# Optimization experiments

Measured on AMD Instinct MI355X. Metric: run time of the kernel, lower is better.

Reference implementation:

```python
import jax, jax.numpy as jnp
import numpy as np

# Fixed production-scale sizes (equal-sized graphs so unbatch == reshape)
B, NQ, ND = 64, 32, 512     # graph pairs, query nodes/graph, data nodes/graph
DIN, D, K = 64, 128, 16     # GCN_in_size, GCN_out_size, NTN_k
DEG = 8                     # average degree


def _gcn(x, src, dst, W, b):
    """GCNConv with self loops + symmetric normalization (PyG semantics)."""
    N = x.shape[0]
    loop = jnp.arange(N)
    s = jnp.concatenate([src, loop])
    t = jnp.concatenate([dst, loop])
    deg = jax.ops.segment_sum(jnp.ones_like(t, x.dtype), t, num_segments=N)
    dinv = jnp.where(deg > 0, deg ** -0.5, 0.0)
    norm = (dinv[s] * dinv[t])[:, None]
    h = x @ W
    return jax.ops.segment_sum(h[s] * norm, t, num_segments=N) + b


def _three_gcn(x, ei, W1, b1, W2, b2, W3, b3):
    src, dst = ei[0], ei[1]
    h1 = jax.nn.relu(_gcn(x, src, dst, W1, b1))
    h2 = jax.nn.relu(_gcn(h1, src, dst, W2, b2))
    h3 = jax.nn.relu(_gcn(h2, src, dst, W3, b3))
    return h1, h2, h3


def _level(q, d, Wn, Vn, bn, cw, cb):
    """att_layer + NTN + elementwise mult + 1x1 conv + softmax over data nodes.
    q: [B,NQ,D], d: [B,ND,D] -> (softmaxed map [B,NQ,ND], raw map, he [B,K,NQ,ND])."""
    att = jax.nn.softmax(jnp.einsum('bqd,bnd->bqn', q, d) / jnp.sqrt(jnp.float32(D)), axis=-1)
    qW = jnp.einsum('bqd,kde->bkqe', q, Wn)           # [B,K,NQ,D]
    bil = jnp.einsum('bkqe,bne->bkqn', qW, d)          # [B,K,NQ,ND]
    lq = jnp.einsum('kd,bqd->bkq', Vn[:, :D], q)[:, :, :, None]
    ld = jnp.einsum('kd,bnd->bkn', Vn[:, D:], d)[:, :, None, :]
    he = jax.nn.sigmoid(bil + lq + ld + bn[None, :, None, None]) * att[:, None]
    e_raw = jnp.einsum('k,bkqn->bqn', cw, he) + cb     # 1x1 Conv2d(K->1)
    return jax.nn.softmax(e_raw, axis=-1), e_raw, he


def reference(x_d, edge_index_d, x_q, edge_index_q, batch_index_d, batch_index_q,
              W1, b1, W2, b2, W3, b3,
              Wn1, Vn1, bn1, cw1, cb1,
              Wn2, Vn2, bn2, cw2, cb2,
              Wn3, Vn3, bn3, cw3, cb3,
              w_end, b_end):
    d1, d2, d3 = _three_gcn(x_d, edge_index_d, W1, b1, W2, b2, W3, b3)
    q1, q2, q3 = _three_gcn(x_q, edge_index_q, W1, b1, W2, b2, W3, b3)
    # unbatch: batch indices are sorted with equal graph sizes -> reshape
    d1, d2, d3 = (t.reshape(B, ND, D) for t in (d1, d2, d3))
    q1, q2, q3 = (t.reshape(B, NQ, D) for t in (q1, q2, q3))
    e1, _, he1 = _level(q1, d1, Wn1, Vn1, bn1, cw1, cb1)
    _, e2raw, he2 = _level(q2, d2, Wn2, Vn2, bn2, cw2, cb2)
    e3, _, he3 = _level(q3, d3, Wn3, Vn3, bn3, cw3, cb3)
    # Faithful to source quirks: the zip unpack `e1,e2,e3,h1,h2,h1` rebinds h1 to
    # he_3 (he_1 is never used, he_3 appears twice) and end2 enters the concat
    # PRE-softmax (the softmaxed version was assigned to unused `nd2`).
    stack = jnp.concatenate([e1[:, None], e2raw[:, None], e3[:, None], he3, he2, he3], axis=1)
    out = jnp.einsum('c,bcqn->bqn', w_end, stack) + b_end  # con_end 1x1 conv + squeeze
    return jax.nn.softmax(out, axis=-1)                    # softmax over data nodes


def setup_inputs() -> dict:
    key = jax.random.key(0)
    k = jax.random.split(key, 40)
    n = jax.random.normal
    Nd, Nq = B * ND, B * NQ
    Ed, Eq = Nd * DEG, Nq * DEG
    gid_d = jnp.repeat(jnp.arange(B), ND * DEG)
    gid_q = jnp.repeat(jnp.arange(B), NQ * DEG)
    inp = {
        'x_d': n(k[0], (Nd, DIN), jnp.float32),
        'x_q': n(k[1], (Nq, DIN), jnp.float32),
        'edge_index_d': jnp.stack([jax.random.randint(k[2], (Ed,), 0, ND) + gid_d * ND,
                                   jax.random.randint(k[3], (Ed,), 0, ND) + gid_d * ND]),
        'edge_index_q': jnp.stack([jax.random.randint(k[4], (Eq,), 0, NQ) + gid_q * NQ,
                                   jax.random.randint(k[5], (Eq,), 0, NQ) + gid_q * NQ]),
        'batch_index_d': jnp.repeat(jnp.arange(B), ND),
        'batch_index_q': jnp.repeat(jnp.arange(B), NQ),
        'W1': n(k[6], (DIN, D), jnp.float32) / np.sqrt(DIN), 'b1': jnp.zeros((D,), jnp.float32),
        'W2': n(k[7], (D, D), jnp.float32) / np.sqrt(D), 'b2': jnp.zeros((D,), jnp.float32),
        'W3': n(k[8], (D, D), jnp.float32) / np.sqrt(D), 'b3': jnp.zeros((D,), jnp.float32),
    }
    for i, l in enumerate(('1', '2', '3')):
        inp['Wn' + l] = n(k[10 + 4 * i], (K, D, D), jnp.float32) / np.sqrt(D)
        inp['Vn' + l] = n(k[11 + 4 * i], (K, 2 * D), jnp.float32) / np.sqrt(2 * D)
        inp['bn' + l] = jnp.zeros((K,), jnp.float32)
        inp['cw' + l] = n(k[12 + 4 * i], (K,), jnp.float32) / np.sqrt(K)
        inp['cb' + l] = jnp.zeros((1,), jnp.float32)
    inp['w_end'] = n(k[25], (3 * K + 3,), jnp.float32) / np.sqrt(3 * K + 3)
    inp['b_end'] = jnp.zeros((1,), jnp.float32)
    return inp
```

## Files before the change

kernel.cpp:

```cpp
#include <hip/hip_runtime.h>
#include <math.h>

namespace {
constexpr int cB  = 64;
constexpr int cNQ = 32;
constexpr int cND = 512;
constexpr int cNd = cB * cND;
constexpr int cNq = cB * cNQ;
constexpr int cEd = cNd * 8;
constexpr int cEq = cNq * 8;
constexpr int LD_STRIDE = 516;
constexpr int NB_CVT = 2188, NB_T2BF = 808, NB_CNT = (cEd + cEq) / 256;
constexpr int NB_FILL = (cEd + cEq) / 256;
}

#define F4C(p) (*(const float4*)(p))

typedef __attribute__((ext_vector_type(8))) __bf16 bf16x8;
typedef __attribute__((ext_vector_type(4))) float floatx4;

__device__ __forceinline__ ushort f2bf(float f) {
  union { float f; unsigned u; } v;
  v.f = f;
  unsigned u = v.u;
  return (ushort)((u + 0x7fffu + ((u >> 16) & 1u)) >> 16);
}
__device__ __forceinline__ float bf2f(ushort u) {
  union { unsigned u; float f; } v;
  v.u = ((unsigned)u) << 16;
  return v.f;
}
__device__ __forceinline__ float4 us4f4(ushort4 u) {
  return make_float4(bf2f(u.x), bf2f(u.y), bf2f(u.z), bf2f(u.w));
}
__device__ __forceinline__ ushort4 f4us4(float4 f) {
  ushort4 o;
  o.x = f2bf(f.x); o.y = f2bf(f.y); o.z = f2bf(f.z); o.w = f2bf(f.w);
  return o;
}
__device__ __forceinline__ float fexp2(float x) {
#if __has_builtin(__builtin_amdgcn_exp2f)
  return __builtin_amdgcn_exp2f(x);
#else
  return exp2f(x);
#endif
}
__device__ __forceinline__ float frcp(float x) {
#if __has_builtin(__builtin_amdgcn_rcpf)
  return __builtin_amdgcn_rcpf(x);
#else
  return 1.0f / x;
#endif
}
__device__ __forceinline__ float fsigmoid(float z) {
  return frcp(1.0f + fexp2(z * -1.4426950408889634f));
}
__device__ __forceinline__ float fexp(float x) { return fexp2(x * 1.4426950408889634f); }

template <int L>
__device__ __forceinline__ int swzg(int j) { return ((j >> (3 + L)) << 3) | (j & 7); }
template <int L>
__device__ __forceinline__ int swzs(int j) { return (j >> 3) & ((1 << L) - 1); }

__global__ __launch_bounds__(256) void k_front(
    const float* __restrict__ xd, const float* __restrict__ xq,
    const float* __restrict__ v0, const float* __restrict__ v1,
    const float* __restrict__ v2, ushort* __restrict__ oxd, ushort* __restrict__ oxq,
    ushort* __restrict__ ov0, ushort* __restrict__ ov1, ushort* __restrict__ ov2,
    const float* __restrict__ W1, const float* __restrict__ W2,
    const float* __restrict__ W3, const float* __restrict__ Wn0,
    const float* __restrict__ Wn1, const float* __restrict__ Wn2,
    ushort* __restrict__ o1, ushort* __restrict__ o2, ushort* __restrict__ o3,
    ushort* __restrict__ on0, ushort* __restrict__ on1, ushort* __restrict__ on2,
    const int* __restrict__ dst_d, const int* __restrict__ dst_q,
    int* __restrict__ cnt_d, int* __restrict__ cnt_q) {
  __shared__ float tile[32][33];
  int blk = blockIdx.x, tid = threadIdx.x;
  if (blk < NB_CVT) {
    const float* src;
    ushort* dst;
    int i;
    if (blk < 2048) { src = xd; dst = oxd; i = blk * 256 + tid; }
    else if (blk < 2176) { src = xq; dst = oxq; i = (blk - 2048) * 256 + tid; }
    else if (blk < 2180) { src = v0; dst = ov0; i = (blk - 2176) * 256 + tid; }
    else if (blk < 2184) { src = v1; dst = ov1; i = (blk - 2180) * 256 + tid; }
    else { src = v2; dst = ov2; i = (blk - 2184) * 256 + tid; }
    *(ushort4*)(dst + (size_t)i * 4) = f4us4(F4C(src + (size_t)i * 4));
  } else if (blk < NB_CVT + NB_T2BF) {
    int b5 = blk - NB_CVT;
    const float* in;
    ushort* out;
    int R, C, bt, t;
    if (b5 < 8)        { in = W1;  out = o1;  R = 64;  C = 128; bt = 0; t = b5; }
    else if (b5 < 24)  { in = W2;  out = o2;  R = 128; C = 128; bt = 0; t = b5 - 8; }
    else if (b5 < 40)  { in = W3;  out = o3;  R = 128; C = 128; bt = 0; t = b5 - 24; }
    else if (b5 < 296) { in = Wn0; out = on0; R = 128; C = 128; bt = (b5 - 40) >> 4;  t = (b5 - 40) & 15; }
    else if (b5 < 552) { in = Wn1; out = on1; R = 128; C = 128; bt = (b5 - 296) >> 4; t = (b5 - 296) & 15; }
    else               { in = Wn2; out = on2; R = 128; C = 128; bt = (b5 - 552) >> 4; t = (b5 - 552) & 15; }
    int tilesC = C >> 5;
    int tr = t / tilesC, tc = t - tr * tilesC;
    int tx = tid & 31, ty = tid >> 5;
    const float* ib = in + (size_t)bt * R * C;
    ushort* ob = out + (size_t)bt * R * C;
#pragma unroll
    for (int i = 0; i < 4; ++i)
      tile[ty + i * 8][tx] = ib[(tr * 32 + ty + i * 8) * C + tc * 32 + tx];
    __syncthreads();
#pragma unroll
    for (int i = 0; i < 4; ++i)
      ob[(size_t)(tc * 32 + ty + i * 8) * R + tr * 32 + tx] = f2bf(tile[tx][ty + i * 8]);
  } else {
    int i = (blk - NB_CVT - NB_T2BF) * 256 + tid;
    if (i < cEd) atomicAdd(&cnt_d[dst_d[i]], 1);
    else atomicAdd(&cnt_q[dst_q[i - cEd]], 1);
  }
}

__global__ __launch_bounds__(512) void k_scan_dinv(
    const int* __restrict__ cnt_d, const int* __restrict__ cnt_q,
    int* __restrict__ rp_d, int* __restrict__ rp_q,
    float* __restrict__ dinv_d, float* __restrict__ dinv_q) {
  __shared__ int sh[512];
  int blk = blockIdx.x, tid = threadIdx.x;
  if (blk < 64) {
    int v = cnt_d[blk * 512 + tid];
    sh[tid] = v;
    __syncthreads();
    for (int off = 1; off < 512; off <<= 1) {
      int t = (tid >= off) ? sh[tid - off] : 0;
      __syncthreads();
      sh[tid] += t;
      __syncthreads();
    }
    rp_d[blk * 512 + tid] = blk * 4096 + sh[tid] - v;
  } else if (blk < 68) {
    int g = (blk - 64) * 16 + (tid >> 5);
    int lane32 = tid & 31;
    int v = cnt_q[g * 32 + lane32];
    int incl = v;
#pragma unroll
    for (int off = 1; off < 32; off <<= 1) {
      int t = __shfl_up(incl, off, 32);
      if (lane32 >= off) incl += t;
    }
    rp_q[g * 32 + lane32] = g * 256 + incl - v;
  } else {
    int i = (blk - 68) * 512 + tid;
    if (i < cNd) dinv_d[i] = 1.0f / sqrtf((float)(cnt_d[i] + 1));
    else dinv_q[i - cNd] = 1.0f / sqrtf((float)(cnt_q[i - cNd] + 1));
  }
}

__global__ __launch_bounds__(256) void k_fill_gemm1(
    const int* __restrict__ src_d, const int* __restrict__ dst_d,
    const int* __restrict__ src_q, const int* __restrict__ dst_q,
    const int* __restrict__ rp_d, const int* __restrict__ rp_q,
    int* __restrict__ cur_d, int* __restrict__ cur_q, int* __restrict__ col_d,
    int* __restrict__ col_q, const ushort* __restrict__ xdbf,
    const ushort* __restrict__ xqbf, const ushort* __restrict__ w1T,
    const float* __restrict__ dinv_d, const float* __restrict__ dinv_q,
    ushort* __restrict__ htmp) {
  int blk = blockIdx.x, tid = threadIdx.x;
  if (blk < NB_FILL) {
    int i = blk * 256 + tid;
    if (i < cEd) {
      int d = dst_d[i];
      int p = atomicAdd(&cur_d[d], 1);
      col_d[rp_d[d] + p] = src_d[i];
    } else {
      int j = i - cEd;
      int d = dst_q[j];
      int p = atomicAdd(&cur_q[d], 1);
      col_q[rp_q[d] + p] = src_q[j];
    }
    return;
  }
  int blk2 = blk - NB_FILL;
  int wave = tid >> 6, lane = tid & 63;
  int col = lane & 15, quad = lane >> 4;
  bool isQ = blk2 >= 512;
  int node0;
  if (isQ) node0 = (blk2 - 512) * 64;
  else node0 = swzg<3>(blk2) * 512 + swzs<3>(blk2) * 64;
  int mloc = node0 + wave * 16;
  const ushort* X = isQ ? xqbf : xdbf;
  const float* dv = isQ ? dinv_q : dinv_d;
  size_t hbase = isQ ? (size_t)cNd : 0;
  floatx4 acc[8];
#pragma unroll
  for (int ct = 0; ct < 8; ++ct)
#pragma unroll
    for (int r = 0; r < 4; ++r) acc[ct][r] = 0.0f;
#pragma unroll
  for (int kc = 0; kc < 2; ++kc) {
    bf16x8 a = *(const bf16x8*)(X + (size_t)(mloc + col) * 64 + kc * 32 + quad * 8);
#pragma unroll
    for (int ct = 0; ct < 8; ++ct) {
      bf16x8 b = *(const bf16x8*)(w1T + (size_t)(ct * 16 + col) * 64 + kc * 32 + quad * 8);
      acc[ct] = __builtin_amdgcn_mfma_f32_16x16x32_bf16(a, b, acc[ct], 0, 0, 0);
    }
  }
  float sc[4];
#pragma unroll
  for (int r = 0; r < 4; ++r) sc[r] = dv[mloc + quad * 4 + r];
#pragma unroll
  for (int ct = 0; ct < 8; ++ct)
#pragma unroll
    for (int r = 0; r < 4; ++r)
      htmp[(hbase + mloc + quad * 4 + r) * 128 + ct * 16 + col] = f2bf(acc[ct][r] * sc[r]);
}

__global__ __launch_bounds__(256) void gmn_gather_merged(
    const ushort* __restrict__ htmp, const int* __restrict__ rp_d,
    const int* __restrict__ cnt_d, const int* __restrict__ col_d,
    const float* __restrict__ dinv_d, const int* __restrict__ rp_q,
    const int* __restrict__ cnt_q, const int* __restrict__ col_q,
    const float* __restrict__ dinv_q, const float* __restrict__ bias,
    ushort* __restrict__ dbf, ushort* __restrict__ qbf) {
  int blk = blockIdx.x, tid = threadIdx.x;
  bool isQ = blk >= 4096;
  int node;
  if (isQ) {
    int j = blk - 4096;
    node = swzg<2>(j) * 32 + swzs<2>(j) * 8 + (tid >> 5);
  } else {
    node = swzg<6>(blk) * 512 + swzs<6>(blk) * 8 + (tid >> 5);
  }
  int l = tid & 31;
  const ushort* hs = htmp + (isQ ? (size_t)cNd * 128 : 0);
  const int* rp = isQ ? rp_q : rp_d;
  const int* cnt = isQ ? cnt_q : cnt_d;
  const int* col = isQ ? col_q : col_d;
  const float* dinv = isQ ? dinv_q : dinv_d;
  ushort* outp = isQ ? qbf : dbf;
  int c = cnt[node], s0 = rp[node];
  float dt = dinv[node];
  float4 acc = us4f4(*(const ushort4*)(hs + (size_t)node * 128 + l * 4));
  int cm = c < 32 ? c : 32;
  for (int j0 = 0; j0 < cm; j0 += 8) {
    int ss[8];
    ushort4 v[8];
#pragma unroll
    for (int t = 0; t < 8; ++t) {
      int jj = j0 + t;
      ss[t] = (jj < cm) ? col[s0 + jj] : -1;
    }
#pragma unroll
    for (int t = 0; t < 8; ++t)
      if (ss[t] >= 0) v[t] = *(const ushort4*)(hs + (size_t)ss[t] * 128 + l * 4);
#pragma unroll
    for (int t = 0; t < 8; ++t) {
      if (ss[t] >= 0) {
        float4 f = us4f4(v[t]);
        acc.x += f.x; acc.y += f.y; acc.z += f.z; acc.w += f.w;
      }
    }
  }
  for (int j = 32; j < c; ++j) {
    int s = col[s0 + j];
    float4 f = us4f4(*(const ushort4*)(hs + (size_t)s * 128 + l * 4));
    acc.x += f.x; acc.y += f.y; acc.z += f.z; acc.w += f.w;
  }
  float4 bv = F4C(bias + l * 4);
  float4 r;
  r.x = fmaxf(acc.x * dt + bv.x, 0.0f);
  r.y = fmaxf(acc.y * dt + bv.y, 0.0f);
  r.z = fmaxf(acc.z * dt + bv.z, 0.0f);
  r.w = fmaxf(acc.w * dt + bv.w, 0.0f);
  *(ushort4*)(outp + (size_t)node * 128 + l * 4) = f4us4(r);
}

__global__ __launch_bounds__(256) void gmn_qw(const ushort* __restrict__ qbf,
                                              const ushort* __restrict__ wnT,
                                              ushort* __restrict__ qw) {
  int blk = blockIdx.x, tid = threadIdx.x;
  int wave = tid >> 6, lane = tid & 63;
  int col = lane & 15, quad = lane >> 4;
  int b = swzg<4>(blk), k = swzs<4>(blk);
  int et0 = wave * 2;
  floatx4 acc[2][2];
#pragma unroll
  for (int qt = 0; qt < 2; ++qt)
#pragma unroll
    for (int ei = 0; ei < 2; ++ei)
#pragma unroll
      for (int r = 0; r < 4; ++r) acc[qt][ei][r] = 0.0f;
#pragma unroll
  for (int kc = 0; kc < 4; ++kc) {
    bf16x8 a0 = *(const bf16x8*)(qbf + (size_t)(b * 32 + col) * 128 + kc * 32 + quad * 8);
    bf16x8 a1 = *(const bf16x8*)(qbf + (size_t)(b * 32 + 16 + col) * 128 + kc * 32 + quad * 8);
#pragma unroll
    for (int ei = 0; ei < 2; ++ei) {
      bf16x8 bf = *(const bf16x8*)(wnT + (size_t)(k * 128 + (et0 + ei) * 16 + col) * 128 +
                                   kc * 32 + quad * 8);
      acc[0][ei] = __builtin_amdgcn_mfma_f32_16x16x32_bf16(a0, bf, acc[0][ei], 0, 0, 0);
      acc[1][ei] = __builtin_amdgcn_mfma_f32_16x16x32_bf16(a1, bf, acc[1][ei], 0, 0, 0);
    }
  }
#pragma unroll
  for (int qt = 0; qt < 2; ++qt)
#pragma unroll
    for (int ei = 0; ei < 2; ++ei)
#pragma unroll
      for (int r = 0; r < 4; ++r)
        qw[((size_t)(b * 16 + k) << 12) + (qt * 16 + quad * 4 + r) * 128 +
           (et0 + ei) * 16 + col] = f2bf(acc[qt][ei][r]);
}

__global__ __launch_bounds__(512, 2) void k_level_gemm(
    const ushort* __restrict__ qbf, const ushort* __restrict__ dbf,
    const ushort* __restrict__ qw, const ushort* __restrict__ vnbf,
    const float* __restrict__ bn, const float* __restrict__ cw,
    const float* __restrict__ w_end, const float* __restrict__ b_end,
    int o1, int o2, int hasF, int do_sm, int mode, int widx,
    float* __restrict__ accb, float* __restrict__ out,
    const ushort* __restrict__ gWT, const float* __restrict__ dinv_d,
    const float* __restrict__ dinv_q, ushort* __restrict__ htmp) {
  __shared__ float s_ld[16 * LD_STRIDE];
  __shared__ float s_lq[16 * 16];
  __shared__ float s_red[16 * 8];
  int tid = threadIdx.x;
  int wave = tid >> 6, lane = tid & 63;
  int col = lane & 15, quad = lane >> 4;

  if (blockIdx.x >= 128) {
    int gblk = blockIdx.x - 128;
    bool isQ = gblk >= 256;
    int node0;
    if (isQ) node0 = (gblk - 256) * 128;
    else node0 = swzg<2>(gblk) * 512 + swzs<2>(gblk) * 128;
    int mloc = node0 + wave * 16;
    const ushort* X = isQ ? qbf : dbf;
    const float* dv = isQ ? dinv_q : dinv_d;
    size_t hbase = isQ ? (size_t)cNd : 0;
    floatx4 acc[8];
#pragma unroll
    for (int ct = 0; ct < 8; ++ct)
#pragma unroll
      for (int r = 0; r < 4; ++r) acc[ct][r] = 0.0f;
#pragma unroll
    for (int kc = 0; kc < 4; ++kc) {
      bf16x8 a = *(const bf16x8*)(X + (size_t)(mloc + col) * 128 + kc * 32 + quad * 8);
#pragma unroll
      for (int ct = 0; ct < 8; ++ct) {
        bf16x8 b = *(const bf16x8*)(gWT + (size_t)(ct * 16 + col) * 128 + kc * 32 + quad * 8);
        acc[ct] = __builtin_amdgcn_mfma_f32_16x16x32_bf16(a, b, acc[ct], 0, 0, 0);
      }
    }
    float sc[4];
#pragma unroll
    for (int r = 0; r < 4; ++r) sc[r] = dv[mloc + quad * 4 + r];
#pragma unroll
    for (int ct = 0; ct < 8; ++ct)
#pragma unroll
      for (int r = 0; r < 4; ++r)
        htmp[(hbase + mloc + quad * 4 + r) * 128 + ct * 16 + col] = f2bf(acc[ct][r] * sc[r]);
    return;
  }

  int b = swzg<1>(blockIdx.x);
  int qh = swzs<1>(blockIdx.x);
  int n0 = wave * 64;

  bf16x8 bfr[4][4];
#pragma unroll
  for (int s = 0; s < 4; ++s)
#pragma unroll
    for (int kc = 0; kc < 4; ++kc)
      bfr[s][kc] = *(const bf16x8*)(dbf + ((size_t)(b * 512 + n0 + s * 16 + col) << 7) +
                                    kc * 32 + quad * 8);
  bf16x8 aq[4];
#pragma unroll
  for (int kc = 0; kc < 4; ++kc)
    aq[kc] = *(const bf16x8*)(qbf + (size_t)(b * 32 + qh * 16 + col) * 128 +
                              kc * 32 + quad * 8);

  floatx4 att[4];
#pragma unroll
  for (int s = 0; s < 4; ++s)
#pragma unroll
    for (int r = 0; r < 4; ++r) att[s][r] = 0.0f;
#pragma unroll
  for (int kc = 0; kc < 4; ++kc)
#pragma unroll
    for (int s = 0; s < 4; ++s)
      att[s] = __builtin_amdgcn_mfma_f32_16x16x32_bf16(aq[kc], bfr[s][kc], att[s], 0, 0, 0);
  const float sc = 0.088388347648318440550f;
#pragma unroll
  for (int s = 0; s < 4; ++s)
#pragma unroll
    for (int r = 0; r < 4; ++r) att[s][r] *= sc;

  {
    bf16x8 vn2[4];
#pragma unroll
    for (int kc = 0; kc < 4; ++kc)
      vn2[kc] = *(const bf16x8*)(vnbf + col * 256 + 128 + kc * 32 + quad * 8);
#pragma unroll
    for (int s = 0; s < 4; ++s) {
      floatx4 lda;
#pragma unroll
      for (int r = 0; r < 4; ++r) lda[r] = 0.0f;
#pragma unroll
      for (int kc = 0; kc < 4; ++kc)
        lda = __builtin_amdgcn_mfma_f32_16x16x32_bf16(bfr[s][kc], vn2[kc], lda, 0, 0, 0);
#pragma unroll
      for (int r = 0; r < 4; ++r)
        s_ld[col * LD_STRIDE + n0 + s * 16 + quad * 4 + r] = lda[r];
    }
  }
  if (wave == 0) {
    bf16x8 vn1[4];
#pragma unroll
    for (int kc = 0; kc < 4; ++kc)
      vn1[kc] = *(const bf16x8*)(vnbf + col * 256 + kc * 32 + quad * 8);
    floatx4 lqa;
#pragma unroll
    for (int r = 0; r < 4; ++r) lqa[r] = 0.0f;
#pragma unroll
    for (int kc = 0; kc < 4; ++kc)
      lqa = __builtin_amdgcn_mfma_f32_16x16x32_bf16(aq[kc], vn1[kc], lqa, 0, 0, 0);
#pragma unroll
    for (int r = 0; r < 4; ++r) s_lq[col * 16 + quad * 4 + r] = lqa[r];
  }
  __syncthreads();

  float red[4], M[4];
#pragma unroll
  for (int r = 0; r < 4; ++r) {
    float m = fmaxf(fmaxf(att[0][r], att[1][r]), fmaxf(att[2][r], att[3][r]));
#pragma unroll
    for (int o = 1; o < 16; o <<= 1) m = fmaxf(m, __shfl_xor(m, o, 64));
    red[r] = m;
  }
  if (col == 0)
#pragma unroll
    for (int r = 0; r < 4; ++r) s_red[(quad * 4 + r) * 8 + wave] = red[r];
  __syncthreads();
#pragma unroll
  for (int r = 0; r < 4; ++r) {
    float m = s_red[(quad * 4 + r) * 8];
#pragma unroll
    for (int w = 1; w < 8; ++w) m = fmaxf(m, s_red[(quad * 4 + r) * 8 + w]);
    M[r] = m;
  }
  __syncthreads();
#pragma unroll
  for (int s = 0; s < 4; ++s)
#pragma unroll
    for (int r = 0; r < 4; ++r) att[s][r] = fexp(att[s][r] - M[r]);
#pragma unroll
  for (int r = 0; r < 4; ++r) {
    float m = att[0][r] + att[1][r] + att[2][r] + att[3][r];
#pragma unroll
    for (int o = 1; o < 16; o <<= 1) m += __shfl_xor(m, o, 64);
    red[r] = m;
  }
  if (col == 0)
#pragma unroll
    for (int r = 0; r < 4; ++r) s_red[(quad * 4 + r) * 8 + wave] = red[r];
  __syncthreads();
#pragma unroll
  for (int r = 0; r < 4; ++r) {
    float m = s_red[(quad * 4 + r) * 8];
#pragma unroll
    for (int w = 1; w < 8; ++w) m += s_red[(quad * 4 + r) * 8 + w];
    M[r] = frcp(m);
  }
  __syncthreads();
#pragma unroll
  for (int s = 0; s < 4; ++s)
#pragma unroll
    for (int r = 0; r < 4; ++r) att[s][r] *= M[r];

  floatx4 eacc[4], facc[4];
#pragma unroll
  for (int s = 0; s < 4; ++s)
#pragma unroll
    for (int r = 0; r < 4; ++r) { eacc[s][r] = 0.0f; facc[s][r] = 0.0f; }

#pragma unroll 4
  for (int k = 0; k < 16; ++k) {
    const ushort* qk = qw + ((size_t)(b * 16 + k) << 12) + (qh * 16 + col) * 128 + quad * 8;
    bf16x8 a0 = *(const bf16x8*)(qk);
    bf16x8 a1 = *(const bf16x8*)(qk + 32);
    bf16x8 a2 = *(const bf16x8*)(qk + 64);
    bf16x8 a3 = *(const bf16x8*)(qk + 96);
    floatx4 bil[4];
#pragma unroll
    for (int s = 0; s < 4; ++s) {
#pragma unroll
      for (int r = 0; r < 4; ++r) bil[s][r] = 0.0f;
      bil[s] = __builtin_amdgcn_mfma_f32_16x16x32_bf16(a0, bfr[s][0], bil[s], 0, 0, 0);
      bil[s] = __builtin_amdgcn_mfma_f32_16x16x32_bf16(a1, bfr[s][1], bil[s], 0, 0, 0);
      bil[s] = __builtin_amdgcn_mfma_f32_16x16x32_bf16(a2, bfr[s][2], bil[s], 0, 0, 0);
      bil[s] = __builtin_amdgcn_mfma_f32_16x16x32_bf16(a3, bfr[s][3], bil[s], 0, 0, 0);
    }
    float bnk = bn[k], cwk = cw[k];
    float wkk = 0.0f;
    if (hasF) {
      wkk = w_end[o1 + k];
      if (o2 >= 0) wkk += w_end[o2 + k];
    }
    float lqv[4];
#pragma unroll
    for (int r = 0; r < 4; ++r) lqv[r] = s_lq[k * 16 + quad * 4 + r] + bnk;
#pragma unroll
    for (int s = 0; s < 4; ++s) {
      float ldv = s_ld[k * LD_STRIDE + n0 + s * 16 + col];
#pragma unroll
      for (int r = 0; r < 4; ++r) {
        float sg = fsigmoid(bil[s][r] + lqv[r] + ldv);
        eacc[s][r] += cwk * sg;
        facc[s][r] += wkk * sg;
      }
    }
  }

#pragma unroll
  for (int s = 0; s < 4; ++s)
#pragma unroll
    for (int r = 0; r < 4; ++r) {
      eacc[s][r] *= att[s][r];
      facc[s][r] *= att[s][r];
    }
  if (do_sm) {
#pragma unroll
    for (int r = 0; r < 4; ++r) {
      float m = fmaxf(fmaxf(eacc[0][r], eacc[1][r]), fmaxf(eacc[2][r], eacc[3][r]));
#pragma unroll
      for (int o = 1; o < 16; o <<= 1) m = fmaxf(m, __shfl_xor(m, o, 64));
      red[r] = m;
    }
    if (col == 0)
#pragma unroll
      for (int r = 0; r < 4; ++r) s_red[(quad * 4 + r) * 8 + wave] = red[r];
    __syncthreads();
#pragma unroll
    for (int r = 0; r < 4; ++r) {
      float m = s_red[(quad * 4 + r) * 8];
#pragma unroll
      for (int w = 1; w < 8; ++w) m = fmaxf(m, s_red[(quad * 4 + r) * 8 + w]);
      M[r] = m;
    }
    __syncthreads();
#pragma unroll
    for (int s = 0; s < 4; ++s)
#pragma unroll
      for (int r = 0; r < 4; ++r) eacc[s][r] = fexp(eacc[s][r] - M[r]);
#pragma unroll
    for (int r = 0; r < 4; ++r) {
      float m = eacc[0][r] + eacc[1][r] + eacc[2][r] + eacc[3][r];
#pragma unroll
      for (int o = 1; o < 16; o <<= 1) m += __shfl_xor(m, o, 64);
      red[r] = m;
    }
    if (col == 0)
#pragma unroll
      for (int r = 0; r < 4; ++r) s_red[(quad * 4 + r) * 8 + wave] = red[r];
    __syncthreads();
#pragma unroll
    for (int r = 0; r < 4; ++r) {
      float m = s_red[(quad * 4 + r) * 8];
#pragma unroll
      for (int w = 1; w < 8; ++w) m += s_red[(quad * 4 + r) * 8 + w];
      M[r] = frcp(m);
    }
    __syncthreads();
#pragma unroll
    for (int s = 0; s < 4; ++s)
#pragma unroll
      for (int r = 0; r < 4; ++r) eacc[s][r] *= M[r];
  }
  float w = w_end[widx];
#pragma unroll
  for (int s = 0; s < 4; ++s)
#pragma unroll
    for (int r = 0; r < 4; ++r) eacc[s][r] = w * eacc[s][r] + (hasF ? facc[s][r] : 0.0f);

  if (mode == 0) {
#pragma unroll
    for (int s = 0; s < 4; ++s)
#pragma unroll
      for (int r = 0; r < 4; ++r)
        accb[((size_t)(b * 32 + qh * 16 + quad * 4 + r) << 9) + n0 + s * 16 + col] =
            eacc[s][r];
  } else if (mode == 1) {
#pragma unroll
    for (int s = 0; s < 4; ++s)
#pragma unroll
      for (int r = 0; r < 4; ++r)
        accb[((size_t)(b * 32 + qh * 16 + quad * 4 + r) << 9) + n0 + s * 16 + col] +=
            eacc[s][r];
  } else {
    float be = b_end[0];
#pragma unroll
    for (int s = 0; s < 4; ++s)
#pragma unroll
      for (int r = 0; r < 4; ++r)
        eacc[s][r] += accb[((size_t)(b * 32 + qh * 16 + quad * 4 + r) << 9) +
                           n0 + s * 16 + col] + be;
#pragma unroll
    for (int r = 0; r < 4; ++r) {
      float m = fmaxf(fmaxf(eacc[0][r], eacc[1][r]), fmaxf(eacc[2][r], eacc[3][r]));
#pragma unroll
      for (int o = 1; o < 16; o <<= 1) m = fmaxf(m, __shfl_xor(m, o, 64));
      red[r] = m;
    }
    if (col == 0)
#pragma unroll
      for (int r = 0; r < 4; ++r) s_red[(quad * 4 + r) * 8 + wave] = red[r];
    __syncthreads();
#pragma unroll
    for (int r = 0; r < 4; ++r) {
      float m = s_red[(quad * 4 + r) * 8];
#pragma unroll
      for (int w2 = 1; w2 < 8; ++w2) m = fmaxf(m, s_red[(quad * 4 + r) * 8 + w2]);
      M[r] = m;
    }
    __syncthreads();
#pragma unroll
    for (int s = 0; s < 4; ++s)
#pragma unroll
      for (int r = 0; r < 4; ++r) eacc[s][r] = fexp(eacc[s][r] - M[r]);
#pragma unroll
    for (int r = 0; r < 4; ++r) {
      float m = eacc[0][r] + eacc[1][r] + eacc[2][r] + eacc[3][r];
#pragma unroll
      for (int o = 1; o < 16; o <<= 1) m += __shfl_xor(m, o, 64);
      red[r] = m;
    }
    if (col == 0)
#pragma unroll
      for (int r = 0; r < 4; ++r) s_red[(quad * 4 + r) * 8 + wave] = red[r];
    __syncthreads();
#pragma unroll
    for (int r = 0; r < 4; ++r) {
      float m = s_red[(quad * 4 + r) * 8];
#pragma unroll
      for (int w2 = 1; w2 < 8; ++w2) m += s_red[(quad * 4 + r) * 8 + w2];
      M[r] = frcp(m);
    }
#pragma unroll
    for (int s = 0; s < 4; ++s)
#pragma unroll
      for (int r = 0; r < 4; ++r)
        out[((size_t)(b * 32 + qh * 16 + quad * 4 + r) << 9) + n0 + s * 16 + col] =
            eacc[s][r] * M[r];
  }
}

extern "C" void kernel_launch(void* const* d_in, const int* in_sizes, int n_in,
                              void* d_out, int out_size, void* d_ws, size_t ws_size,
                              hipStream_t stream) {
  (void)in_sizes; (void)n_in; (void)out_size; (void)ws_size;
  const float* x_d = (const float*)d_in[0];
  const float* x_q = (const float*)d_in[1];
  const int* ei_d = (const int*)d_in[2];
  const int* ei_q = (const int*)d_in[3];
  const float* W1 = (const float*)d_in[6];
  const float* b1 = (const float*)d_in[7];
  const float* W2 = (const float*)d_in[8];
  const float* b2 = (const float*)d_in[9];
  const float* W3 = (const float*)d_in[10];
  const float* b3 = (const float*)d_in[11];
  const float* Wn[3] = {(const float*)d_in[12], (const float*)d_in[17], (const float*)d_in[22]};
  const float* Vn[3] = {(const float*)d_in[13], (const float*)d_in[18], (const float*)d_in[23]};
  const float* bn[3] = {(const float*)d_in[14], (const float*)d_in[19], (const float*)d_in[24]};
  const float* cw[3] = {(const float*)d_in[15], (const float*)d_in[20], (const float*)d_in[25]};
  const float* w_end = (const float*)d_in[27];
  const float* b_end = (const float*)d_in[28];
  float* out = (float*)d_out;

  char* wsp = (char*)d_ws;
  auto alloc = [&](size_t nbytes) {
    void* p = (void*)wsp;
    wsp += (nbytes + 255) & ~(size_t)255;
    return p;
  };
  int* cnt_d = (int*)alloc(cNd * 4);
  int* cnt_q = (int*)alloc(cNq * 4);
  int* cur_d = (int*)alloc(cNd * 4);
  int* cur_q = (int*)alloc(cNq * 4);
  float* dinv_d = (float*)alloc(cNd * 4);
  float* dinv_q = (float*)alloc(cNq * 4);
  int* rp_d = (int*)alloc(cNd * 4);
  int* rp_q = (int*)alloc(cNq * 4);
  int* col_d = (int*)alloc((size_t)cEd * 4);
  int* col_q = (int*)alloc((size_t)cEq * 4);
  ushort* xdbf = (ushort*)alloc((size_t)cNd * 64 * 2);
  ushort* xqbf = (ushort*)alloc((size_t)cNq * 64 * 2);
  ushort* w1T = (ushort*)alloc(128 * 64 * 2);
  ushort* w2T = (ushort*)alloc(128 * 128 * 2);
  ushort* w3T = (ushort*)alloc(128 * 128 * 2);
  ushort* wnT[3];
  for (int l = 0; l < 3; ++l) wnT[l] = (ushort*)alloc((size_t)16 * 128 * 128 * 2);
  ushort* vnbf[3];
  for (int l = 0; l < 3; ++l) vnbf[l] = (ushort*)alloc(16 * 256 * 2);
  ushort* htmp = (ushort*)alloc((size_t)(cNd + cNq) * 128 * 2);
  ushort* dbf = (ushort*)alloc((size_t)cNd * 128 * 2);
  ushort* qbf[3];
  for (int l = 0; l < 3; ++l) qbf[l] = (ushort*)alloc((size_t)cNq * 128 * 2);
  float* accb = (float*)alloc((size_t)cB * cNQ * cND * 4);
  ushort* qwbuf = (ushort*)alloc((size_t)cB * 16 * 32 * 128 * 2);

  const int* src_d = ei_d;
  const int* dst_d = ei_d + cEd;
  const int* src_q = ei_q;
  const int* dst_q = ei_q + cEq;

  hipMemsetAsync(cnt_d, 0, (size_t)2 * (cNd + cNq) * 4, stream);

  k_front<<<NB_CVT + NB_T2BF + NB_CNT, 256, 0, stream>>>(
      x_d, x_q, Vn[0], Vn[1], Vn[2], xdbf, xqbf, vnbf[0], vnbf[1], vnbf[2], W1, W2,
      W3, Wn[0], Wn[1], Wn[2], w1T, w2T, w3T, wnT[0], wnT[1], wnT[2], dst_d, dst_q,
      cnt_d, cnt_q);

  k_scan_dinv<<<136, 512, 0, stream>>>(cnt_d, cnt_q, rp_d, rp_q, dinv_d, dinv_q);

  k_fill_gemm1<<<NB_FILL + 544, 256, 0, stream>>>(
      src_d, dst_d, src_q, dst_q, rp_d, rp_q, cur_d, cur_q, col_d, col_q, xdbf, xqbf,
      w1T, dinv_d, dinv_q, htmp);

  const float* bias[3] = {b1, b2, b3};
  const ushort* nextWT[3] = {w2T, w3T, nullptr};
  const int o1s[3] = {0, 19, 3};
  const int o2s[3] = {-1, -1, 35};
  const int hasF[3] = {0, 1, 1};
  const int dosms[3] = {1, 0, 1};
  const int modes[3] = {0, 1, 2};

  for (int l = 0; l < 3; ++l) {
    gmn_gather_merged<<<(cNd + cNq) / 8, 256, 0, stream>>>(
        htmp, rp_d, cnt_d, col_d, dinv_d, rp_q, cnt_q, col_q, dinv_q, bias[l], dbf,
        qbf[l]);
    gmn_qw<<<1024, 256, 0, stream>>>(qbf[l], wnT[l], qwbuf);
    int grid = (l < 2) ? (128 + 272) : 128;
    k_level_gemm<<<grid, 512, 0, stream>>>(
        qbf[l], dbf, qwbuf, vnbf[l], bn[l], cw[l], w_end, b_end, o1s[l], o2s[l],
        hasF[l], dosms[l], modes[l], l, accb, out, nextWT[l], dinv_d, dinv_q, htmp);
  }
}
```

Before: 301.6 us.

## Stage each graph's feature rows in LDS for GCN neighbor gather

The GCN aggregation kernel now uses 136 large blocks of 512 threads. Each block copies a whole 512-row slab of transformed features (128 KB) into dynamic shared memory, then aggregates neighbors for 256 nodes out of LDS instead of through scattered global loads. This works because edges stay inside each graph, so every neighbor falls inside the slab. The cost is far fewer blocks than CUs, a serial loop of 16 nodes per thread group, and each slab being loaded twice by paired blocks.

```diff
diff --git a/kernel.cpp b/kernel.cpp
--- a/kernel.cpp
+++ b/kernel.cpp
@@ -12,6 +12,7 @@
 constexpr int LD_STRIDE = 516;
 constexpr int NB_CVT = 2188, NB_T2BF = 808, NB_CNT = (cEd + cEq) / 256;
 constexpr int NB_FILL = (cEd + cEq) / 256;
+constexpr size_t GATHER_LDS = 512 * 128 * 2;
 }
 
 #define F4C(p) (*(const float4*)(p))
@@ -210,64 +211,76 @@
       htmp[(hbase + mloc + quad * 4 + r) * 128 + ct * 16 + col] = f2bf(acc[ct][r] * sc[r]);
 }
 
-__global__ __launch_bounds__(256) void gmn_gather_merged(
+__global__ __launch_bounds__(512) void gmn_gather_lds(
     const ushort* __restrict__ htmp, const int* __restrict__ rp_d,
     const int* __restrict__ cnt_d, const int* __restrict__ col_d,
-    const float* __restrict__ dinv_d, const int* __restrict__ rp_q,
-    const int* __restrict__ cnt_q, const int* __restrict__ col_q,
+    const int* __restrict__ rp_q, const int* __restrict__ cnt_q,
+    const int* __restrict__ col_q, const float* __restrict__ dinv_d,
     const float* __restrict__ dinv_q, const float* __restrict__ bias,
     ushort* __restrict__ dbf, ushort* __restrict__ qbf) {
+  extern __shared__ ushort s_rows[];
   int blk = blockIdx.x, tid = threadIdx.x;
-  bool isQ = blk >= 4096;
-  int node;
+  bool isQ = blk >= 128;
+  int row0, node0;
+  const ushort* hs;
+  const int *rp, *cnt, *col;
+  const float* dinv;
+  ushort* outp;
   if (isQ) {
-    int j = blk - 4096;
-    node = swzg<2>(j) * 32 + swzs<2>(j) * 8 + (tid >> 5);
+    int j = blk - 128;
+    row0 = (j >> 1) * 512;
+    node0 = row0 + (j & 1) * 256;
+    hs = htmp + (size_t)cNd * 128;
+    rp = rp_q; cnt = cnt_q; col = col_q; dinv = dinv_q; outp = qbf;
   } else {
-    node = swzg<6>(blk) * 512 + swzs<6>(blk) * 8 + (tid >> 5);
-  }
+    row0 = (blk >> 1) * 512;
+    node0 = row0 + (blk & 1) * 256;
+    hs = htmp;
+    rp = rp_d; cnt = cnt_d; col = col_d; dinv = dinv_d; outp = dbf;
+  }
+  {
+    const float4* src = (const float4*)(hs + (size_t)row0 * 128);
+    float4* dst = (float4*)s_rows;
+#pragma unroll
+    for (int i = 0; i < 16; ++i) dst[tid + 512 * i] = src[tid + 512 * i];
+  }
+  __syncthreads();
   int l = tid & 31;
-  const ushort* hs = htmp + (isQ ? (size_t)cNd * 128 : 0);
-  const int* rp = isQ ? rp_q : rp_d;
-  const int* cnt = isQ ? cnt_q : cnt_d;
-  const int* col = isQ ? col_q : col_d;
-  const float* dinv = isQ ? dinv_q : dinv_d;
-  ushort* outp = isQ ? qbf : dbf;
-  int c = cnt[node], s0 = rp[node];
-  float dt = dinv[node];
-  float4 acc = us4f4(*(const ushort4*)(hs + (size_t)node * 128 + l * 4));
-  int cm = c < 32 ? c : 32;
-  for (int j0 = 0; j0 < cm; j0 += 8) {
-    int ss[8];
-    ushort4 v[8];
-#pragma unroll
-    for (int t = 0; t < 8; ++t) {
-      int jj = j0 + t;
-      ss[t] = (jj < cm) ? col[s0 + jj] : -1;
-    }
-#pragma unroll
-    for (int t = 0; t < 8; ++t)
-      if (ss[t] >= 0) v[t] = *(const ushort4*)(hs + (size_t)ss[t] * 128 + l * 4);
-#pragma unroll
-    for (int t = 0; t < 8; ++t) {
-      if (ss[t] >= 0) {
-        float4 f = us4f4(v[t]);
-        acc.x += f.x; acc.y += f.y; acc.z += f.z; acc.w += f.w;
+  int grp = tid >> 5;
+  for (int it = 0; it < 16; ++it) {
+    int node = node0 + it * 16 + grp;
+    int c = cnt[node], s0 = rp[node];
+    float dt = dinv[node];
+    float4 acc = us4f4(*(const ushort4*)(s_rows + (size_t)(node - row0) * 128 + l * 4));
+    int cm = c < 32 ? c : 32;
+    for (int j0 = 0; j0 < cm; j0 += 8) {
+      int ss[8];
+#pragma unroll
+      for (int t = 0; t < 8; ++t) {
+        int jj = j0 + t;
+        ss[t] = (jj < cm) ? (col[s0 + jj] - row0) : -1;
       }
-    }
-  }
-  for (int j = 32; j < c; ++j) {
-    int s = col[s0 + j];
-    float4 f = us4f4(*(const ushort4*)(hs + (size_t)s * 128 + l * 4));
-    acc.x += f.x; acc.y += f.y; acc.z += f.z; acc.w += f.w;
-  }
-  float4 bv = F4C(bias + l * 4);
-  float4 r;
-  r.x = fmaxf(acc.x * dt + bv.x, 0.0f);
-  r.y = fmaxf(acc.y * dt + bv.y, 0.0f);
-  r.z = fmaxf(acc.z * dt + bv.z, 0.0f);
-  r.w = fmaxf(acc.w * dt + bv.w, 0.0f);
-  *(ushort4*)(outp + (size_t)node * 128 + l * 4) = f4us4(r);
+#pragma unroll
+      for (int t = 0; t < 8; ++t) {
+        if (ss[t] >= 0) {
+          float4 f = us4f4(*(const ushort4*)(s_rows + (size_t)ss[t] * 128 + l * 4));
+          acc.x += f.x; acc.y += f.y; acc.z += f.z; acc.w += f.w;
+        }
+      }
+    }
+    for (int j = 32; j < c; ++j) {
+      int s = col[s0 + j] - row0;
+      float4 f = us4f4(*(const ushort4*)(s_rows + (size_t)s * 128 + l * 4));
+      acc.x += f.x; acc.y += f.y; acc.z += f.z; acc.w += f.w;
+    }
+    float4 bv = F4C(bias + l * 4);
+    float4 r;
+    r.x = fmaxf(acc.x * dt + bv.x, 0.0f);
+    r.y = fmaxf(acc.y * dt + bv.y, 0.0f);
+    r.z = fmaxf(acc.z * dt + bv.z, 0.0f);
+    r.w = fmaxf(acc.w * dt + bv.w, 0.0f);
+    *(ushort4*)(outp + (size_t)node * 128 + l * 4) = f4us4(r);
+  }
 }
 
 __global__ __launch_bounds__(256) void gmn_qw(const ushort* __restrict__ qbf,
@@ -671,6 +684,10 @@
   const float* w_end = (const float*)d_in[27];
   const float* b_end = (const float*)d_in[28];
   float* out = (float*)d_out;
+
+  (void)hipFuncSetAttribute((const void*)gmn_gather_lds,
+                            hipFuncAttributeMaxDynamicSharedMemorySize,
+                            (int)GATHER_LDS);
 
   char* wsp = (char*)d_ws;
   auto alloc = [&](size_t nbytes) {
@@ -731,8 +748,8 @@
   const int modes[3] = {0, 1, 2};
 
   for (int l = 0; l < 3; ++l) {
-    gmn_gather_merged<<<(cNd + cNq) / 8, 256, 0, stream>>>(
-        htmp, rp_d, cnt_d, col_d, dinv_d, rp_q, cnt_q, col_q, dinv_q, bias[l], dbf,
+    gmn_gather_lds<<<136, 512, GATHER_LDS, stream>>>(
+        htmp, rp_d, cnt_d, col_d, rp_q, cnt_q, col_q, dinv_d, dinv_q, bias[l], dbf,
         qbf[l]);
     gmn_qw<<<1024, 256, 0, stream>>>(qbf[l], wnT[l], qwbuf);
     int grid = (l < 2) ? (128 + 272) : 128;
```

After: 393.9 us. +30.6%, slower.
